# Optimization experiments

Hardware: AMD Instinct MI355X
Metric: run time of the kernel (lower is better)

Reference implementation:

```python
import jax, jax.numpy as jnp
import numpy as np

B_SZ, L, D_MODEL = 2, 1024, 1024
EXPAND, D_STATE, D_CONV = 2, 16, 4
D_INNER = D_MODEL * EXPAND
DT_RANK = max(D_MODEL // 16, 1)


def setup_inputs() -> dict:
    key = jax.random.key(0)
    ks = jax.random.split(key, 9)
    s = 0.02
    x = jax.random.normal(ks[0], (B_SZ, L, D_MODEL), jnp.float32)
    W_in = jax.random.normal(ks[1], (2 * D_INNER, D_MODEL), jnp.float32) * s
    conv_w = jax.random.normal(ks[2], (D_INNER, D_CONV), jnp.float32) * 0.1
    conv_b = jax.random.normal(ks[3], (D_INNER,), jnp.float32) * 0.01
    W_x = jax.random.normal(ks[4], (DT_RANK + 2 * D_STATE, D_INNER), jnp.float32) * s
    W_dt = jax.random.normal(ks[5], (D_INNER, DT_RANK), jnp.float32) * s
    b_dt = jax.random.normal(ks[6], (D_INNER,), jnp.float32) * 0.01
    A_log = jnp.log(jnp.broadcast_to(jnp.arange(1, D_STATE + 1, dtype=jnp.float32), (D_INNER, D_STATE)))
    D_param = jnp.ones((D_INNER,), jnp.float32)
    W_out = jax.random.normal(ks[7], (D_MODEL, D_INNER), jnp.float32) * s
    return {"x": x, "W_in": W_in, "conv_w": conv_w, "conv_b": conv_b,
            "W_x": W_x, "W_dt": W_dt, "b_dt": b_dt, "A_log": A_log,
            "D_param": D_param, "W_out": W_out}


def _mamba_fwd(x, W_in, conv_w, conv_b, W_x, W_dt, b_dt, A_log, D_param, W_out):
    # in-proj and gate split
    xz = jnp.einsum("bld,ed->ble", x, W_in)            # (B, L, 2*d_inner)
    x_ssm, z = jnp.split(xz, 2, axis=-1)
    # causal depthwise 1D conv (left pad d_conv-1 == torch pad-both + [:L])
    xc = x_ssm.transpose(0, 2, 1)                        # (B, d_inner, L)
    xc = jax.lax.conv_general_dilated(
        xc, conv_w[:, None, :], window_strides=(1,),
        padding=[(D_CONV - 1, 0)], feature_group_count=D_INNER,
        dimension_numbers=("NCH", "OIH", "NCH"))
    xc = xc + conv_b[None, :, None]
    x_ssm = jax.nn.silu(xc.transpose(0, 2, 1))           # (B, L, d_inner)
    # input-dependent dt, B, C
    dbc = jnp.einsum("bld,ed->ble", x_ssm, W_x)
    dt, B_sel, C_sel = jnp.split(dbc, [DT_RANK, DT_RANK + D_STATE], axis=-1)
    delta = jax.nn.softplus(jnp.einsum("blr,dr->bld", dt, W_dt) + b_dt)
    A = -jnp.exp(A_log)                                  # (d_inner, d_state)
    # discretization
    deltaA = jnp.exp(delta[..., None] * A)               # (B, L, d_inner, d_state)
    dBu = delta[..., None] * B_sel[:, :, None, :] * x_ssm[..., None]
    # linear recurrence h_t = deltaA_t * h_{t-1} + dBu_t via associative scan
    def comb(e1, e2):
        a1, b1 = e1
        a2, b2 = e2
        return (a1 * a2, a2 * b1 + b2)
    _, h = jax.lax.associative_scan(comb, (deltaA, dBu), axis=1)
    y = jnp.sum(h * C_sel[:, :, None, :], axis=-1)       # (B, L, d_inner)
    y = y + x_ssm * D_param
    y = y * jax.nn.silu(z)
    return jnp.einsum("ble,de->bld", y, W_out)


def reference(x, W_in, conv_w, conv_b, W_x, W_dt, b_dt, A_log, D_param, W_out):
    return _mamba_fwd(x, W_in, conv_w, conv_b, W_x, W_dt, b_dt, A_log, D_param, W_out)
```

## Files before the change

### kernel.cpp

```cpp
#include <hip/hip_runtime.h>
#include <hip/hip_bf16.h>

#define B_SZ   2
#define SEQ    1024
#define DMODEL 1024
#define DINNER 2048
#define DSTATE 16
#define DCONV  4
#define DTRANK 64
#define BLROWS (B_SZ*SEQ)
#define NCHUNK 32
#define TCHUNK (SEQ/NCHUNK)
#define NSLICE 16
#define LOG2E 1.44269504088896f

using floatx4 = __attribute__((ext_vector_type(4))) float;
using short8  = __attribute__((ext_vector_type(8))) short;
using us8     = __attribute__((ext_vector_type(8))) unsigned short;
using us4     = __attribute__((ext_vector_type(4))) unsigned short;

__device__ __forceinline__ float softplus_f(float x) {
    return fmaxf(x, 0.f) + log1pf(__expf(-fabsf(x)));
}
__device__ __forceinline__ float silu_f(float x) {
    return x / (1.f + __expf(-x));
}
__device__ __forceinline__ short bfs(float x) {
    union { __hip_bfloat16 h; short s; } u;
    u.h = __float2bfloat16(x);
    return u.s;
}
__device__ __forceinline__ float b2f(unsigned short s) {
    union { float f; unsigned u; } x;
    x.u = ((unsigned)s) << 16;
    return x.f;
}
__device__ __forceinline__ void gld16(const void* g, void* l) {
    __builtin_amdgcn_global_load_lds((const __attribute__((address_space(1))) void*)g,
                                     (__attribute__((address_space(3))) void*)l,
                                     16, 0, 0);
}
__device__ __forceinline__ void cast8(const float* src, unsigned short* dst, int i) {
    const float* p = src + (size_t)i*8;
    float4 a = *(const float4*)p, b = *(const float4*)(p+4);
    us8 o;
    o[0]=(unsigned short)bfs(a.x); o[1]=(unsigned short)bfs(a.y);
    o[2]=(unsigned short)bfs(a.z); o[3]=(unsigned short)bfs(a.w);
    o[4]=(unsigned short)bfs(b.x); o[5]=(unsigned short)bfs(b.y);
    o[6]=(unsigned short)bfs(b.z); o[7]=(unsigned short)bfs(b.w);
    *(us8*)(dst + (size_t)i*8) = o;
}

#define G0 (BLROWS*DMODEL/8)
#define G1 (2*DINNER*DMODEL/8)
#define G2 (96*DINNER/8)
#define G3 (DINNER*DTRANK/8)
#define G4 (DMODEL*DINNER/8)
#define GTOT (G0+G1+G2+G3+G4)
__global__ __launch_bounds__(256)
void init_kernel(const float* __restrict__ x, const float* __restrict__ W_in,
                 const float* __restrict__ W_x, const float* __restrict__ W_dt,
                 const float* __restrict__ W_out,
                 unsigned short* xH, unsigned short* WinH, unsigned short* WxH,
                 unsigned short* WdtH, unsigned short* WoutH)
{
    int i = blockIdx.x*256 + threadIdx.x;
    if (i < G0) { cast8(x, xH, i); return; }            i -= G0;
    if (i < G1) { cast8(W_in, WinH, i); return; }       i -= G1;
    if (i < G2) { cast8(W_x, WxH, i); return; }         i -= G2;
    if (i < G3) { cast8(W_dt, WdtH, i); return; }       i -= G3;
    if (i < G4) { cast8(W_out, WoutH, i); }
}

template<int TM, int TN, int EPI, bool NGUARD>
__global__ __launch_bounds__(256)
void gemm_tn(const __hip_bfloat16* __restrict__ Ag, const __hip_bfloat16* __restrict__ Bg,
             int M, int N, int K, int kslice,
             float* __restrict__ outF,
             __hip_bfloat16* __restrict__ outH,
             __hip_bfloat16* __restrict__ outH2,
             const float* __restrict__ bias)
{
    constexpr int AG  = TM/64;
    constexpr int EB  = TN/64;
    constexpr int MF  = TM/32;
    constexpr int NF  = TN/32;
    __shared__ short As[2][TM*32];
    __shared__ short Bs[2][TN*32];

    const int tid  = threadIdx.x;
    const int lane = tid & 63, wave = tid >> 6;
    const int bm0  = blockIdx.x * TM;
    const int bn0  = blockIdx.y * TN;
    const int kbeg = blockIdx.z * kslice;
    const int kend = kbeg + kslice;
    const int wrow = (wave >> 1) * (TM/2), wcol = (wave & 1) * (TN/2);
    const int lrow = lane & 15, quad = lane >> 4;

    const int srow = wave*16 + (lane >> 2);
    const int scol = (lane & 3) * 8;

    const __hip_bfloat16* ga0 = Ag + (size_t)(bm0 + srow)*K      + scol;
    const __hip_bfloat16* ga1 = (AG > 1) ? Ag + (size_t)(bm0 + srow + 64)*K + scol : nullptr;
    const __hip_bfloat16* gb0 = Bg + (size_t)(bn0 + srow)*K      + scol;
    const __hip_bfloat16* gb1 = (EB > 1) ? Bg + (size_t)(bn0 + srow + 64)*K + scol : nullptr;
    const bool b0ok = !NGUARD || (bn0 + wave*16) < N;
    const bool b1ok = (EB > 1) && (!NGUARD || (bn0 + wave*16 + 64) < N);

    auto stage = [&](int c, int k0) {
        gld16(ga0 + k0, &As[c][(wave*16)*32]);
        if (AG > 1) gld16(ga1 + k0, &As[c][(wave*16 + 64)*32]);
        if (b0ok) gld16(gb0 + k0, &Bs[c][(wave*16)*32]);
        if (EB > 1 && b1ok) gld16(gb1 + k0, &Bs[c][(wave*16 + 64)*32]);
    };

    floatx4 acc[MF][NF] = {};

    stage(0, kbeg);
    __syncthreads();
    int cur = 0;
    for (int k0 = kbeg; k0 < kend; k0 += 32) {
        if (k0 + 32 < kend) stage(cur ^ 1, k0 + 32);
        short8 af[MF], bf[NF];
        #pragma unroll
        for (int i = 0; i < MF; i++)
            af[i] = *(const short8*)&As[cur][(wrow + i*16 + lrow)*32 + quad*8];
        #pragma unroll
        for (int j = 0; j < NF; j++)
            bf[j] = *(const short8*)&Bs[cur][(wcol + j*16 + lrow)*32 + quad*8];
        #pragma unroll
        for (int i = 0; i < MF; i++)
            #pragma unroll
            for (int j = 0; j < NF; j++)
                acc[i][j] = __builtin_amdgcn_mfma_f32_16x16x32_bf16(af[i], bf[j], acc[i][j], 0, 0, 0);
        __syncthreads();
        cur ^= 1;
    }

    const int rq = quad * 4;
    #pragma unroll
    for (int i = 0; i < MF; i++) {
        #pragma unroll
        for (int j = 0; j < NF; j++) {
            int col = bn0 + wcol + j*16 + lrow;
            if (NGUARD && col >= N) continue;
            if constexpr (EPI == 8) {
                int row0 = bm0 + wrow + i*16 + rq;
                int bb = row0 >> 10, ll = row0 & (SEQ-1);
                us4 pk;
                #pragma unroll
                for (int r = 0; r < 4; r++)
                    pk[r] = (unsigned short)bfs(softplus_f(acc[i][j][r] + bias[col]));
                *(us4*)((unsigned short*)outH + ((size_t)bb*DINNER + col)*SEQ + ll) = pk;
            } else {
                #pragma unroll
                for (int r = 0; r < 4; r++) {
                    int row = bm0 + wrow + i*16 + rq + r;
                    float v = acc[i][j][r];
                    if constexpr (EPI == 5) {
                        if (col < DINNER)
                            outH[(size_t)row*DINNER + col] = __float2bfloat16(v);
                        else
                            outH2[(size_t)row*DINNER + (col - DINNER)] = __float2bfloat16(v);
                    } else if constexpr (EPI == 9) {
                        outF[(size_t)blockIdx.z*M*N + (size_t)row*N + col] = v;
                    }
                }
            }
        }
    }
}

__global__ __launch_bounds__(192)
void dbc_reduce_kernel(const float* __restrict__ part, float* __restrict__ dbc,
                       __hip_bfloat16* __restrict__ dtH)
{
    const int tid = threadIdx.x;
    const int r2  = (tid >= 96) ? 1 : 0;
    const int col = tid - 96*r2;
    const int row = blockIdx.x*2 + r2;
    const size_t idx = (size_t)row*96 + col;
    float s = 0.f;
    #pragma unroll
    for (int z = 0; z < NSLICE; z++)
        s += part[(size_t)z*(BLROWS*96) + idx];
    dbc[idx] = s;
    if (col < DTRANK)
        dtH[(size_t)row*DTRANK + col] = __float2bfloat16(s);
}

__global__ __launch_bounds__(256)
void conv_transpose_kernel(const unsigned short* __restrict__ xbufN,
                           const float* __restrict__ cw,
                           const float* __restrict__ cb,
                           unsigned short* __restrict__ xsN,
                           unsigned short* __restrict__ xsT)
{
    __shared__ unsigned short t[67*68];
    __shared__ unsigned short t2[64*68];
    const int tid = threadIdx.x;
    const int l0 = blockIdx.x * 64, d0 = blockIdx.y * 64, b = blockIdx.z;

    const int lc4 = (tid & 15) * 4;
    for (int r = tid >> 4; r < 67; r += 16) {
        int lg = l0 - 3 + r;
        us4 v = {0,0,0,0};
        if (lg >= 0)
            v = *(const us4*)&xbufN[((size_t)(b*SEQ + lg))*DINNER + d0 + lc4];
        *(us4*)&t[r*68 + lc4] = v;
    }
    __syncthreads();

    const int dd = tid & 63;
    float4 w4 = *(const float4*)&cw[(d0 + dd)*4];
    float  bb = cb[d0 + dd];
    #pragma unroll 4
    for (int rr = tid >> 6; rr < 64; rr += 4) {
        float acc = bb;
        acc += w4.x * b2f(t[(rr+0)*68 + dd]);
        acc += w4.y * b2f(t[(rr+1)*68 + dd]);
        acc += w4.z * b2f(t[(rr+2)*68 + dd]);
        acc += w4.w * b2f(t[(rr+3)*68 + dd]);
        unsigned short h = (unsigned short)bfs(silu_f(acc));
        t2[rr*68 + dd] = h;
        xsN[((size_t)(b*SEQ + l0 + rr))*DINNER + d0 + dd] = h;
    }
    __syncthreads();

    const int dr = tid >> 4, lc = tid & 15;
    #pragma unroll
    for (int i = 0; i < 4; i++) {
        int dT = dr + i*16;
        us4 w;
        #pragma unroll
        for (int j = 0; j < 4; j++)
            w[j] = t2[(lc*4 + j)*68 + dT];
        *(us4*)&xsT[((size_t)b*DINNER + d0 + dT)*SEQ + l0 + lc*4] = w;
    }
}

__global__ __launch_bounds__(256)
void scan_pass1(const unsigned short* __restrict__ deT,
                const unsigned short* __restrict__ xsT,
                const float* __restrict__ dbc,
                const float* __restrict__ A_log,
                float* __restrict__ Bc, float* __restrict__ sde)
{
    __shared__ float bs[TCHUNK*16];
    const int tid  = threadIdx.x;
    const int q    = tid & 3, dsub = tid >> 2;
    const int blk  = blockIdx.x;
    const int dg   = blk & 31;
    const int c    = (blk >> 5) & (NCHUNK-1);
    const int b    = blk >> 10;
    const int d    = dg*64 + dsub;

    size_t b96 = (size_t)b*SEQ*96;
    if (tid < TCHUNK*4) {
        int r = tid >> 2, f = (tid & 3) * 4;
        *(float4*)&bs[r*16 + f] =
            *(const float4*)&dbc[b96 + (size_t)(c*TCHUNK + r)*96 + DTRANK + f];
    }

    float An[4];
    *(float4*)An = *(const float4*)&A_log[d*DSTATE + 4*q];
    bool okv = true;
    #pragma unroll
    for (int j = 0; j < 4; j++) {
        An[j] = -__expf(An[j]) * LOG2E;
        okv = okv && (fabsf(An[j] + (float)(4*q + j + 1) * LOG2E) < 2e-3f * (float)(4*q + j + 1));
    }
    const bool fast = __all((int)okv);

    size_t rowT = ((size_t)b*DINNER + d)*SEQ;
    __syncthreads();

    float h[4] = {0.f,0.f,0.f,0.f};
    float s = 0.f;
    if (fast) {
        for (int t8 = 0; t8 < TCHUNK/8; ++t8) {
            int l0 = c*TCHUNK + t8*8;
            us8 de8 = *(const us8*)&deT[rowT + l0];
            us8 u8  = *(const us8*)&xsT[rowT + l0];
            #pragma unroll
            for (int j2 = 0; j2 < 8; j2++) {
                int lr = t8*8 + j2;
                float Bn[4];
                *(float4*)Bn = *(const float4*)&bs[lr*16 + 4*q];
                float de = b2f(de8[j2]);
                float du = de * b2f(u8[j2]);
                float r  = exp2f(de * (-LOG2E));
                float r2 = r*r, r4 = r2*r2, r8 = r4*r4;
                float rb = ((q & 2) ? r8 : 1.0f) * ((q & 1) ? r4 : 1.0f);
                float e0 = rb*r, e1 = e0*r, e2 = e1*r, e3 = e2*r;
                h[0] = e0*h[0] + du*Bn[0];
                h[1] = e1*h[1] + du*Bn[1];
                h[2] = e2*h[2] + du*Bn[2];
                h[3] = e3*h[3] + du*Bn[3];
                s += de;
            }
        }
    } else {
        for (int t8 = 0; t8 < TCHUNK/8; ++t8) {
            int l0 = c*TCHUNK + t8*8;
            us8 de8 = *(const us8*)&deT[rowT + l0];
            us8 u8  = *(const us8*)&xsT[rowT + l0];
            #pragma unroll
            for (int j2 = 0; j2 < 8; j2++) {
                int lr = t8*8 + j2;
                float Bn[4];
                *(float4*)Bn = *(const float4*)&bs[lr*16 + 4*q];
                float de = b2f(de8[j2]);
                float du = de * b2f(u8[j2]);
                #pragma unroll
                for (int j = 0; j < 4; j++)
                    h[j] = exp2f(de*An[j])*h[j] + du*Bn[j];
                s += de;
            }
        }
    }
    size_t ci = (size_t)(b*NCHUNK + c)*DINNER + d;
    *(float4*)&Bc[ci*16 + 4*q] = *(float4*)h;
    if (q == 0) sde[ci] = s;
}

__global__ __launch_bounds__(256)
void scan_pass2(float* __restrict__ Bc, const float* __restrict__ sde,
                const float* __restrict__ A_log)
{
    const int tid = threadIdx.x;
    const int n   = tid & 15, dl = tid >> 4;
    const int blk = blockIdx.x;
    const int dg  = blk & 127, b = blk >> 7;
    const int d   = dg*16 + dl;
    const float An = -__expf(A_log[d*DSTATE + n]) * LOG2E;

    float H = 0.f;
    for (int c = 0; c < NCHUNK; ++c) {
        size_t ci = (size_t)(b*NCHUNK + c)*DINNER + d;
        float bc = Bc[ci*16 + n];
        Bc[ci*16 + n] = H;
        H = exp2f(An*sde[ci])*H + bc;
    }
}

__global__ __launch_bounds__(256)
void scan_pass3(const unsigned short* __restrict__ deT,
                const unsigned short* __restrict__ xsT,
                const float* __restrict__ dbc,
                const float* __restrict__ A_log,
                const float* __restrict__ Dp,
                const float* __restrict__ Hinit,
                const unsigned short* __restrict__ zN,
                __hip_bfloat16* __restrict__ yN)
{
    __shared__ float bcs[TCHUNK*32];
    const int tid  = threadIdx.x;
    const int q    = tid & 3, dsub = tid >> 2;
    const int blk  = blockIdx.x;
    const int dg   = blk & 31;
    const int c    = (blk >> 5) & (NCHUNK-1);
    const int b    = blk >> 10;
    const int d    = dg*64 + dsub;

    size_t b96 = (size_t)b*SEQ*96;
    {
        int r = tid >> 3, f = (tid & 7) * 4;
        *(float4*)&bcs[r*32 + f] =
            *(const float4*)&dbc[b96 + (size_t)(c*TCHUNK + r)*96 + DTRANK + f];
    }

    float An[4];
    *(float4*)An = *(const float4*)&A_log[d*DSTATE + 4*q];
    bool okv = true;
    #pragma unroll
    for (int j = 0; j < 4; j++) {
        An[j] = -__expf(An[j]) * LOG2E;
        okv = okv && (fabsf(An[j] + (float)(4*q + j + 1) * LOG2E) < 2e-3f * (float)(4*q + j + 1));
    }
    const bool fast = __all((int)okv);
    const float Dd = Dp[d];

    size_t rowT  = ((size_t)b*DINNER + d)*SEQ;
    size_t baseN = (size_t)b*SEQ*DINNER + d;

    float h[4];
    *(float4*)h = *(const float4*)&Hinit[((size_t)(b*NCHUNK + c)*DINNER + d)*16 + 4*q];
    __syncthreads();

    if (fast) {
        for (int t8 = 0; t8 < TCHUNK/8; ++t8) {
            int l0 = c*TCHUNK + t8*8;
            us8 de8 = *(const us8*)&deT[rowT + l0];
            us8 u8  = *(const us8*)&xsT[rowT + l0];
            #pragma unroll
            for (int j2 = 0; j2 < 8; j2++) {
                int l  = l0 + j2;
                int lr = t8*8 + j2;
                float Bn[4], Cn[4];
                *(float4*)Bn = *(const float4*)&bcs[lr*32 + 4*q];
                *(float4*)Cn = *(const float4*)&bcs[lr*32 + 16 + 4*q];
                float de = b2f(de8[j2]);
                float u  = b2f(u8[j2]);
                float du = de * u;
                float r  = exp2f(de * (-LOG2E));
                float r2 = r*r, r4 = r2*r2, r8 = r4*r4;
                float rb = ((q & 2) ? r8 : 1.0f) * ((q & 1) ? r4 : 1.0f);
                float e0 = rb*r, e1 = e0*r, e2 = e1*r, e3 = e2*r;
                h[0] = e0*h[0] + du*Bn[0];
                h[1] = e1*h[1] + du*Bn[1];
                h[2] = e2*h[2] + du*Bn[2];
                h[3] = e3*h[3] + du*Bn[3];
                float cc = h[0]*Cn[0] + h[1]*Cn[1] + h[2]*Cn[2] + h[3]*Cn[3];
                cc += __shfl_xor(cc, 1);
                cc += __shfl_xor(cc, 2);
                if (q == 0) {
                    float zv = silu_f(b2f(zN[baseN + (size_t)l*DINNER]));
                    yN[baseN + (size_t)l*DINNER] = __float2bfloat16((cc + u*Dd) * zv);
                }
            }
        }
    } else {
        for (int t8 = 0; t8 < TCHUNK/8; ++t8) {
            int l0 = c*TCHUNK + t8*8;
            us8 de8 = *(const us8*)&deT[rowT + l0];
            us8 u8  = *(const us8*)&xsT[rowT + l0];
            #pragma unroll
            for (int j2 = 0; j2 < 8; j2++) {
                int l  = l0 + j2;
                int lr = t8*8 + j2;
                float Bn[4], Cn[4];
                *(float4*)Bn = *(const float4*)&bcs[lr*32 + 4*q];
                *(float4*)Cn = *(const float4*)&bcs[lr*32 + 16 + 4*q];
                float de = b2f(de8[j2]);
                float u  = b2f(u8[j2]);
                float du = de * u;
                float cc = 0.f;
                #pragma unroll
                for (int j = 0; j < 4; j++) {
                    h[j] = exp2f(de*An[j])*h[j] + du*Bn[j];
                    cc += h[j]*Cn[j];
                }
                cc += __shfl_xor(cc, 1);
                cc += __shfl_xor(cc, 2);
                if (q == 0) {
                    float zv = silu_f(b2f(zN[baseN + (size_t)l*DINNER]));
                    yN[baseN + (size_t)l*DINNER] = __float2bfloat16((cc + u*Dd) * zv);
                }
            }
        }
    }
}

__global__ __launch_bounds__(256)
void zero_out_kernel(float* out, int n) {
    int i = blockIdx.x * 256 + threadIdx.x;
    if (i < n) out[i] = 0.f;
}

extern "C" void kernel_launch(void* const* d_in, const int* in_sizes, int n_in,
                              void* d_out, int out_size, void* d_ws, size_t ws_size,
                              hipStream_t stream) {
    const float* x      = (const float*)d_in[0];
    const float* W_in   = (const float*)d_in[1];
    const float* conv_w = (const float*)d_in[2];
    const float* conv_b = (const float*)d_in[3];
    const float* W_x    = (const float*)d_in[4];
    const float* W_dt   = (const float*)d_in[5];
    const float* b_dt   = (const float*)d_in[6];
    const float* A_log  = (const float*)d_in[7];
    const float* D_par  = (const float*)d_in[8];
    const float* W_out  = (const float*)d_in[9];

    size_t szBig = (size_t)BLROWS * DINNER * 2;
    size_t szBc  = (size_t)B_SZ * NCHUNK * DINNER * DSTATE * 4;
    size_t need  = 5*szBig
                 + (size_t)BLROWS*96*4
                 + (size_t)NSLICE*BLROWS*96*4
                 + (size_t)BLROWS*DTRANK*2
                 + szBc + (size_t)B_SZ*NCHUNK*DINNER*4
                 + (size_t)BLROWS*DMODEL*2
                 + (size_t)2*DINNER*DMODEL*2
                 + (size_t)128*DINNER*2
                 + (size_t)DINNER*DTRANK*2
                 + (size_t)DMODEL*DINNER*2;

    if (ws_size < need) {
        zero_out_kernel<<<(out_size + 255)/256, 256, 0, stream>>>((float*)d_out, out_size);
        return;
    }

    char* w = (char*)d_ws;
    __hip_bfloat16* xbufN = (__hip_bfloat16*)w;  w += szBig;
    __hip_bfloat16* zbufN = (__hip_bfloat16*)w;  w += szBig;
    __hip_bfloat16* xsN   = (__hip_bfloat16*)w;  w += szBig;
    __hip_bfloat16* xsT   = (__hip_bfloat16*)w;  w += szBig;
    __hip_bfloat16* deT   = (__hip_bfloat16*)w;  w += szBig;
    float*          dbc   = (float*)w;           w += (size_t)BLROWS * 96 * 4;
    float*          dbcP  = (float*)w;           w += (size_t)NSLICE * BLROWS * 96 * 4;
    __hip_bfloat16* dtH   = (__hip_bfloat16*)w;  w += (size_t)BLROWS * DTRANK * 2;
    float*          Bc    = (float*)w;           w += szBc;
    float*          sde   = (float*)w;           w += (size_t)B_SZ * NCHUNK * DINNER * 4;
    __hip_bfloat16* xH    = (__hip_bfloat16*)w;  w += (size_t)BLROWS*DMODEL*2;
    __hip_bfloat16* WinH  = (__hip_bfloat16*)w;  w += (size_t)2*DINNER*DMODEL*2;
    __hip_bfloat16* WxH   = (__hip_bfloat16*)w;  w += (size_t)128*DINNER*2;
    __hip_bfloat16* WdtH  = (__hip_bfloat16*)w;  w += (size_t)DINNER*DTRANK*2;
    __hip_bfloat16* WoutH = (__hip_bfloat16*)w;  w += (size_t)DMODEL*DINNER*2;
    __hip_bfloat16* yN    = xsN;

    init_kernel<<<GTOT/256, 256, 0, stream>>>(x, W_in, W_x, W_dt, W_out,
        (unsigned short*)xH, (unsigned short*)WinH, (unsigned short*)WxH,
        (unsigned short*)WdtH, (unsigned short*)WoutH);

    gemm_tn<128,128,5,false><<<dim3(BLROWS/128, (2*DINNER)/128, 1), 256, 0, stream>>>(
        xH, WinH, BLROWS, 2*DINNER, DMODEL, DMODEL, nullptr, xbufN, zbufN, nullptr);

    conv_transpose_kernel<<<dim3(SEQ/64, DINNER/64, B_SZ), 256, 0, stream>>>(
        (const unsigned short*)xbufN, conv_w, conv_b,
        (unsigned short*)xsN, (unsigned short*)xsT);

    gemm_tn<128,64,9,true><<<dim3(BLROWS/128, 2, NSLICE), 256, 0, stream>>>(
        xsN, WxH, BLROWS, 96, DINNER, DINNER/NSLICE, dbcP, nullptr, nullptr, nullptr);
    dbc_reduce_kernel<<<BLROWS/2, 192, 0, stream>>>(dbcP, dbc, dtH);

    gemm_tn<128,64,8,false><<<dim3(BLROWS/128, DINNER/64, 1), 256, 0, stream>>>(
        dtH, WdtH, BLROWS, DINNER, DTRANK, DTRANK, nullptr, deT, nullptr, b_dt);

    scan_pass1<<<B_SZ*NCHUNK*32, 256, 0, stream>>>((const unsigned short*)deT,
        (const unsigned short*)xsT, dbc, A_log, Bc, sde);
    scan_pass2<<<B_SZ*128, 256, 0, stream>>>(Bc, sde, A_log);
    scan_pass3<<<B_SZ*NCHUNK*32, 256, 0, stream>>>((const unsigned short*)deT,
        (const unsigned short*)xsT, dbc, A_log, D_par, Bc,
        (const unsigned short*)zbufN, yN);

    gemm_tn<64,64,9,false><<<dim3(BLROWS/64, DMODEL/64, 1), 256, 0, stream>>>(
        yN, WoutH, BLROWS, DMODEL, DINNER, DINNER, (float*)d_out, nullptr, nullptr, nullptr);
}
```

Baseline: 233.3 us.

## Scan with one thread per channel holding all 16 states, dropping shuffles

Scan passes 1 and 3 now give each thread a whole channel with all 16 state elements in registers, instead of four threads sharing a channel with four states each. The per-step cross-lane shuffle reduction and the q==0 write predicate go away, and B/C are read straight from global (uniform across the block, broadcast through cache) instead of being staged in shared memory. The grid shrinks by four times. In exchange each thread uses more registers and there are fewer waves to hide latency, while uncoalesced strided reads of deT/xsT rows per thread stay the same.

```diff
diff --git a/kernel.cpp b/kernel.cpp
--- a/kernel.cpp
+++ b/kernel.cpp
@@ -246,37 +246,30 @@
                 const float* __restrict__ A_log,
                 float* __restrict__ Bc, float* __restrict__ sde)
 {
-    __shared__ float bs[TCHUNK*16];
-    const int tid  = threadIdx.x;
-    const int q    = tid & 3, dsub = tid >> 2;
-    const int blk  = blockIdx.x;
-    const int dg   = blk & 31;
-    const int c    = (blk >> 5) & (NCHUNK-1);
-    const int b    = blk >> 10;
-    const int d    = dg*64 + dsub;
-
-    size_t b96 = (size_t)b*SEQ*96;
-    if (tid < TCHUNK*4) {
-        int r = tid >> 2, f = (tid & 3) * 4;
-        *(float4*)&bs[r*16 + f] =
-            *(const float4*)&dbc[b96 + (size_t)(c*TCHUNK + r)*96 + DTRANK + f];
-    }
-
-    float An[4];
-    *(float4*)An = *(const float4*)&A_log[d*DSTATE + 4*q];
+    const int tid = threadIdx.x;
+    const int blk = blockIdx.x;
+    const int dg  = blk & 7;
+    const int c   = (blk >> 3) & (NCHUNK-1);
+    const int b   = blk >> 8;
+    const int d   = dg*256 + tid;
+
+    float An[16];
     bool okv = true;
     #pragma unroll
-    for (int j = 0; j < 4; j++) {
-        An[j] = -__expf(An[j]) * LOG2E;
-        okv = okv && (fabsf(An[j] + (float)(4*q + j + 1) * LOG2E) < 2e-3f * (float)(4*q + j + 1));
+    for (int n = 0; n < 16; n++) {
+        An[n] = -__expf(A_log[d*DSTATE + n]) * LOG2E;
+        okv = okv && (fabsf(An[n] + (float)(n+1)*LOG2E) < 2e-3f*(float)(n+1));
     }
     const bool fast = __all((int)okv);
 
     size_t rowT = ((size_t)b*DINNER + d)*SEQ;
-    __syncthreads();
-
-    float h[4] = {0.f,0.f,0.f,0.f};
+    const float* brow = dbc + (size_t)b*SEQ*96 + (size_t)(c*TCHUNK)*96 + DTRANK;
+
+    float h[16];
+    #pragma unroll
+    for (int n = 0; n < 16; n++) h[n] = 0.f;
     float s = 0.f;
+
     if (fast) {
         for (int t8 = 0; t8 < TCHUNK/8; ++t8) {
             int l0 = c*TCHUNK + t8*8;
@@ -284,19 +277,16 @@
             us8 u8  = *(const us8*)&xsT[rowT + l0];
             #pragma unroll
             for (int j2 = 0; j2 < 8; j2++) {
-                int lr = t8*8 + j2;
-                float Bn[4];
-                *(float4*)Bn = *(const float4*)&bs[lr*16 + 4*q];
+                const float* br = brow + (size_t)(t8*8 + j2)*96;
                 float de = b2f(de8[j2]);
                 float du = de * b2f(u8[j2]);
                 float r  = exp2f(de * (-LOG2E));
-                float r2 = r*r, r4 = r2*r2, r8 = r4*r4;
-                float rb = ((q & 2) ? r8 : 1.0f) * ((q & 1) ? r4 : 1.0f);
-                float e0 = rb*r, e1 = e0*r, e2 = e1*r, e3 = e2*r;
-                h[0] = e0*h[0] + du*Bn[0];
-                h[1] = e1*h[1] + du*Bn[1];
-                h[2] = e2*h[2] + du*Bn[2];
-                h[3] = e3*h[3] + du*Bn[3];
+                float e  = r;
+                #pragma unroll
+                for (int n = 0; n < 16; n++) {
+                    h[n] = e*h[n] + du*br[n];
+                    e *= r;
+                }
                 s += de;
             }
         }
@@ -307,21 +297,24 @@
             us8 u8  = *(const us8*)&xsT[rowT + l0];
             #pragma unroll
             for (int j2 = 0; j2 < 8; j2++) {
-                int lr = t8*8 + j2;
-                float Bn[4];
-                *(float4*)Bn = *(const float4*)&bs[lr*16 + 4*q];
+                const float* br = brow + (size_t)(t8*8 + j2)*96;
                 float de = b2f(de8[j2]);
                 float du = de * b2f(u8[j2]);
                 #pragma unroll
-                for (int j = 0; j < 4; j++)
-                    h[j] = exp2f(de*An[j])*h[j] + du*Bn[j];
+                for (int n = 0; n < 16; n++)
+                    h[n] = exp2f(de*An[n])*h[n] + du*br[n];
                 s += de;
             }
         }
     }
+
     size_t ci = (size_t)(b*NCHUNK + c)*DINNER + d;
-    *(float4*)&Bc[ci*16 + 4*q] = *(float4*)h;
-    if (q == 0) sde[ci] = s;
+    #pragma unroll
+    for (int n = 0; n < 16; n += 4) {
+        float4 v; v.x = h[n]; v.y = h[n+1]; v.z = h[n+2]; v.w = h[n+3];
+        *(float4*)&Bc[ci*16 + n] = v;
+    }
+    sde[ci] = s;
 }
 
 __global__ __launch_bounds__(256)
@@ -354,39 +347,34 @@
                 const unsigned short* __restrict__ zN,
                 __hip_bfloat16* __restrict__ yN)
 {
-    __shared__ float bcs[TCHUNK*32];
-    const int tid  = threadIdx.x;
-    const int q    = tid & 3, dsub = tid >> 2;
-    const int blk  = blockIdx.x;
-    const int dg   = blk & 31;
-    const int c    = (blk >> 5) & (NCHUNK-1);
-    const int b    = blk >> 10;
-    const int d    = dg*64 + dsub;
-
-    size_t b96 = (size_t)b*SEQ*96;
-    {
-        int r = tid >> 3, f = (tid & 7) * 4;
-        *(float4*)&bcs[r*32 + f] =
-            *(const float4*)&dbc[b96 + (size_t)(c*TCHUNK + r)*96 + DTRANK + f];
-    }
-
-    float An[4];
-    *(float4*)An = *(const float4*)&A_log[d*DSTATE + 4*q];
+    const int tid = threadIdx.x;
+    const int blk = blockIdx.x;
+    const int dg  = blk & 7;
+    const int c   = (blk >> 3) & (NCHUNK-1);
+    const int b   = blk >> 8;
+    const int d   = dg*256 + tid;
+
+    float An[16];
     bool okv = true;
     #pragma unroll
-    for (int j = 0; j < 4; j++) {
-        An[j] = -__expf(An[j]) * LOG2E;
-        okv = okv && (fabsf(An[j] + (float)(4*q + j + 1) * LOG2E) < 2e-3f * (float)(4*q + j + 1));
+    for (int n = 0; n < 16; n++) {
+        An[n] = -__expf(A_log[d*DSTATE + n]) * LOG2E;
+        okv = okv && (fabsf(An[n] + (float)(n+1)*LOG2E) < 2e-3f*(float)(n+1));
     }
     const bool fast = __all((int)okv);
     const float Dd = Dp[d];
 
     size_t rowT  = ((size_t)b*DINNER + d)*SEQ;
     size_t baseN = (size_t)b*SEQ*DINNER + d;
-
-    float h[4];
-    *(float4*)h = *(const float4*)&Hinit[((size_t)(b*NCHUNK + c)*DINNER + d)*16 + 4*q];
-    __syncthreads();
+    const float* brow = dbc + (size_t)b*SEQ*96 + (size_t)(c*TCHUNK)*96 + DTRANK;
+
+    size_t ci = (size_t)(b*NCHUNK + c)*DINNER + d;
+    float h[16];
+    #pragma unroll
+    for (int n = 0; n < 16; n += 4) {
+        float4 v = *(const float4*)&Hinit[ci*16 + n];
+        h[n] = v.x; h[n+1] = v.y; h[n+2] = v.z; h[n+3] = v.w;
+    }
 
     if (fast) {
         for (int t8 = 0; t8 < TCHUNK/8; ++t8) {
@@ -395,29 +383,21 @@
             us8 u8  = *(const us8*)&xsT[rowT + l0];
             #pragma unroll
             for (int j2 = 0; j2 < 8; j2++) {
-                int l  = l0 + j2;
-                int lr = t8*8 + j2;
-                float Bn[4], Cn[4];
-                *(float4*)Bn = *(const float4*)&bcs[lr*32 + 4*q];
-                *(float4*)Cn = *(const float4*)&bcs[lr*32 + 16 + 4*q];
+                int l = l0 + j2;
+                const float* br = brow + (size_t)(t8*8 + j2)*96;
                 float de = b2f(de8[j2]);
                 float u  = b2f(u8[j2]);
                 float du = de * u;
                 float r  = exp2f(de * (-LOG2E));
-                float r2 = r*r, r4 = r2*r2, r8 = r4*r4;
-                float rb = ((q & 2) ? r8 : 1.0f) * ((q & 1) ? r4 : 1.0f);
-                float e0 = rb*r, e1 = e0*r, e2 = e1*r, e3 = e2*r;
-                h[0] = e0*h[0] + du*Bn[0];
-                h[1] = e1*h[1] + du*Bn[1];
-                h[2] = e2*h[2] + du*Bn[2];
-                h[3] = e3*h[3] + du*Bn[3];
-                float cc = h[0]*Cn[0] + h[1]*Cn[1] + h[2]*Cn[2] + h[3]*Cn[3];
-                cc += __shfl_xor(cc, 1);
-                cc += __shfl_xor(cc, 2);
-                if (q == 0) {
-                    float zv = silu_f(b2f(zN[baseN + (size_t)l*DINNER]));
-                    yN[baseN + (size_t)l*DINNER] = __float2bfloat16((cc + u*Dd) * zv);
+                float e  = r, cc = 0.f;
+                #pragma unroll
+                for (int n = 0; n < 16; n++) {
+                    h[n] = e*h[n] + du*br[n];
+                    cc  += h[n]*br[DSTATE + n];
+                    e   *= r;
                 }
+                float zv = silu_f(b2f(zN[baseN + (size_t)l*DINNER]));
+                yN[baseN + (size_t)l*DINNER] = __float2bfloat16((cc + u*Dd) * zv);
             }
         }
     } else {
@@ -427,26 +407,19 @@
             us8 u8  = *(const us8*)&xsT[rowT + l0];
             #pragma unroll
             for (int j2 = 0; j2 < 8; j2++) {
-                int l  = l0 + j2;
-                int lr = t8*8 + j2;
-                float Bn[4], Cn[4];
-                *(float4*)Bn = *(const float4*)&bcs[lr*32 + 4*q];
-                *(float4*)Cn = *(const float4*)&bcs[lr*32 + 16 + 4*q];
+                int l = l0 + j2;
+                const float* br = brow + (size_t)(t8*8 + j2)*96;
                 float de = b2f(de8[j2]);
                 float u  = b2f(u8[j2]);
                 float du = de * u;
                 float cc = 0.f;
                 #pragma unroll
-                for (int j = 0; j < 4; j++) {
-                    h[j] = exp2f(de*An[j])*h[j] + du*Bn[j];
-                    cc += h[j]*Cn[j];
+                for (int n = 0; n < 16; n++) {
+                    h[n] = exp2f(de*An[n])*h[n] + du*br[n];
+                    cc  += h[n]*br[DSTATE + n];
                 }
-                cc += __shfl_xor(cc, 1);
-                cc += __shfl_xor(cc, 2);
-                if (q == 0) {
-                    float zv = silu_f(b2f(zN[baseN + (size_t)l*DINNER]));
-                    yN[baseN + (size_t)l*DINNER] = __float2bfloat16((cc + u*Dd) * zv);
-                }
+                float zv = silu_f(b2f(zN[baseN + (size_t)l*DINNER]));
+                yN[baseN + (size_t)l*DINNER] = __float2bfloat16((cc + u*Dd) * zv);
             }
         }
     }
@@ -526,10 +499,10 @@
     gemm_tn<128,64,8,false><<<dim3(BLROWS/128, DINNER/64, 1), 256, 0, stream>>>(
         dtH, WdtH, BLROWS, DINNER, DTRANK, DTRANK, nullptr, deT, nullptr, b_dt);
 
-    scan_pass1<<<B_SZ*NCHUNK*32, 256, 0, stream>>>((const unsigned short*)deT,
+    scan_pass1<<<B_SZ*NCHUNK*8, 256, 0, stream>>>((const unsigned short*)deT,
         (const unsigned short*)xsT, dbc, A_log, Bc, sde);
     scan_pass2<<<B_SZ*128, 256, 0, stream>>>(Bc, sde, A_log);
-    scan_pass3<<<B_SZ*NCHUNK*32, 256, 0, stream>>>((const unsigned short*)deT,
+    scan_pass3<<<B_SZ*NCHUNK*8, 256, 0, stream>>>((const unsigned short*)deT,
         (const unsigned short*)xsT, dbc, A_log, D_par, Bc,
         (const unsigned short*)zbufN, yN);
 
```

New measurement: 229.8 us. Within noise of the previous version (-1.5%).
